# Optimization experiments

Hardware: AMD Instinct MI355X
Metric: run time of the kernel (lower is better)

The kernel has to match this reference:

```python
import jax, jax.numpy as jnp
import numpy as np

DIM, NH, HD = 1536, 12, 128
F, H, W = 1, 30, 52
SEQ = F * H * W          # 1560 tokens per AR group
NG, GI = 6, 5            # num_groups, group_idx (attend over full prefix)
POS, EPS = 1024, 1e-6


def _rope_table():
    # cos/sin table matching Wan rope_params: bands [c-2(c//3), c//3, c//3] of head_dim//2
    c = HD // 2
    parts = [c - 2 * (c // 3), c // 3, c // 3]
    pos = np.arange(POS, dtype=np.float64)
    angs = []
    for cp in parts:
        inv = 1.0 / (10000.0 ** (np.arange(cp, dtype=np.float64) / cp))
        angs.append(pos[:, None] * inv[None, :])
    ang = np.concatenate(angs, axis=1)  # [POS, c]
    return jnp.asarray(np.stack([np.cos(ang), np.sin(ang)], axis=-1), dtype=jnp.float32)


def setup_inputs() -> dict:
    key = jax.random.key(0)
    ks = jax.random.split(key, 8)
    lin = lambda k: jax.random.normal(k, (DIM, DIM), jnp.float32) * 0.02
    total = NG * SEQ
    return {
        'x': jax.random.normal(ks[0], (1, SEQ, DIM), jnp.float32),
        'wq': lin(ks[1]), 'bq': jnp.zeros((DIM,), jnp.float32),
        'wk': lin(ks[2]), 'bk': jnp.zeros((DIM,), jnp.float32),
        'wv': lin(ks[3]), 'bv': jnp.zeros((DIM,), jnp.float32),
        'wo': lin(ks[4]), 'bo': jnp.zeros((DIM,), jnp.float32),
        'nq_w': jnp.ones((DIM,), jnp.float32),
        'nk_w': jnp.ones((DIM,), jnp.float32),
        'freqs': _rope_table(),
        'k_cache': jax.random.normal(ks[5], (1, total, NH, HD), jnp.float32) * 0.5,
        'v_cache': jax.random.normal(ks[6], (1, total, NH, HD), jnp.float32) * 0.5,
        'f': F, 'h': H, 'w': W, 'group_idx': GI, 'num_groups': NG,
    }


def _rms_norm(x, weight, eps=EPS):
    # fast_rms_norm: normalize over the full channel dim, then scale
    x = x.astype(jnp.float32)
    return x * jax.lax.rsqrt(jnp.mean(x * x, axis=-1, keepdims=True) + eps) * weight


def _rope_apply(x, freqs, f, h, w, group_idx):
    # x: [B, S, N, D] with S = f*h*w; freqs: [POS, D//2, 2] (cos, sin)
    B, S, N, D = x.shape
    c = D // 2
    cf = c - 2 * (c // 3)
    ch = cw = c // 3
    sf = group_idx * f
    fp = jnp.broadcast_to(freqs[sf:sf + f, :cf][:, None, None], (f, h, w, cf, 2))
    hp = jnp.broadcast_to(freqs[:h, cf:cf + ch][None, :, None], (f, h, w, ch, 2))
    wp = jnp.broadcast_to(freqs[:w, cf + ch:][None, None, :], (f, h, w, cw, 2))
    rot = jnp.concatenate([fp, hp, wp], axis=3).reshape(S, c, 2)  # [S, c, 2]
    cos = rot[..., 0][None, :, None]  # [1, S, 1, c]
    sin = rot[..., 1][None, :, None]
    xr = x.astype(jnp.float32).reshape(B, S, N, c, 2)
    out_r = xr[..., 0] * cos - xr[..., 1] * sin  # complex multiply x * e^{i theta}
    out_i = xr[..., 0] * sin + xr[..., 1] * cos
    return jnp.stack([out_r, out_i], axis=-1).reshape(B, S, N, D)


def reference(x, wq, bq, wk, bk, wv, bv, wo, bo, nq_w, nk_w, freqs,
              k_cache, v_cache, f, h, w, group_idx, num_groups):
    B, S, C = x.shape
    n, d = NH, C // NH
    q = _rms_norm(x @ wq.T + bq, nq_w).reshape(B, S, n, d)
    k = _rms_norm(x @ wk.T + bk, nk_w).reshape(B, S, n, d)
    v = (x @ wv.T + bv).reshape(B, S, n, d)
    q = _rope_apply(q, freqs, f, h, w, group_idx)
    k = _rope_apply(k, freqs, f, h, w, group_idx)
    # KV-cache scatter (detached in the original) then prefix gather
    start = group_idx * S
    kc = jax.lax.dynamic_update_slice(k_cache, jax.lax.stop_gradient(k), (0, start, 0, 0))
    vc = jax.lax.dynamic_update_slice(v_cache, jax.lax.stop_gradient(v), (0, start, 0, 0))
    k_full = kc[:, :start + S]  # [B, Lkv, n, d]
    v_full = vc[:, :start + S]
    att = jnp.einsum('bqnd,bknd->bnqk', q, k_full) / jnp.sqrt(jnp.float32(d))
    p = jax.nn.softmax(att, axis=-1)
    o = jnp.einsum('bnqk,bknd->bqnd', p, v_full).reshape(B, S, C)
    return o @ wo.T + bo
```

## Files before the change

kernel.cpp:

```cpp
#include <hip/hip_runtime.h>

#define DIM 1536
#define NH 12
#define HD 128
#define KSPLIT 8
#define KT 32
#define MFIX 3.0f
#define KK48 48

typedef _Float16 half2_t __attribute__((ext_vector_type(2)));
typedef _Float16 half8_t __attribute__((ext_vector_type(8)));
typedef float f32x4 __attribute__((ext_vector_type(4)));

__device__ __forceinline__ half2_t pkrtz(float a, float b) {
    return __builtin_bit_cast(half2_t, __builtin_amdgcn_cvt_pkrtz(a, b));
}

__device__ __forceinline__ void split8(float4 a, float4 b, half8_t& h, half8_t& l) {
    half2_t h0 = pkrtz(a.x, a.y), h1 = pkrtz(a.z, a.w);
    half2_t h2 = pkrtz(b.x, b.y), h3 = pkrtz(b.z, b.w);
    half2_t g0 = pkrtz(a.x - (float)h0.x, a.y - (float)h0.y);
    half2_t g1 = pkrtz(a.z - (float)h1.x, a.w - (float)h1.y);
    half2_t g2 = pkrtz(b.x - (float)h2.x, b.y - (float)h2.y);
    half2_t g3 = pkrtz(b.z - (float)h3.x, b.w - (float)h3.y);
    h[0]=h0.x; h[1]=h0.y; h[2]=h1.x; h[3]=h1.y; h[4]=h2.x; h[5]=h2.y; h[6]=h3.x; h[7]=h3.y;
    l[0]=g0.x; l[1]=g0.y; l[2]=g1.x; l[3]=g1.y; l[4]=g2.x; l[5]=g2.y; l[6]=g3.x; l[7]=g3.y;
}

__device__ __forceinline__ half8_t cvt8rn(float4 a, float4 b) {
    half8_t h;
    h[0]=(_Float16)a.x; h[1]=(_Float16)a.y; h[2]=(_Float16)a.z; h[3]=(_Float16)a.w;
    h[4]=(_Float16)b.x; h[5]=(_Float16)b.y; h[6]=(_Float16)b.z; h[7]=(_Float16)b.w;
    return h;
}

__device__ __forceinline__ void gl2lds16(const void* g, void* l) {
    __builtin_amdgcn_global_load_lds(
        (const __attribute__((address_space(1))) unsigned int*)g,
        (__attribute__((address_space(3))) unsigned int*)(unsigned int)(uintptr_t)l,
        16, 0, 0);
}


__global__ __launch_bounds__(256) void cvt_a_fl(
    const float* __restrict__ src, _Float16* __restrict__ h, _Float16* __restrict__ l,
    int M, int nrec8)
{
    const int i = blockIdx.x * 256 + threadIdx.x;
    if (i >= nrec8) return;
    const int lane = i & 63;
    const int grp  = (i >> 6) & 7;
    const int tile = i >> 9;
    const int kk = tile % KK48, mt = tile / KK48;
    const int row = mt * 128 + grp * 16 + (lane & 15);
    const int k   = kk * 32 + (lane >> 4) * 8;
    float4 a = make_float4(0,0,0,0), b = a;
    if (row < M) {
        const float* s = src + (size_t)row * DIM + k;
        a = *(const float4*)s; b = *(const float4*)(s + 4);
    }
    half8_t hh, ll; split8(a, b, hh, ll);
    ((half8_t*)h)[i] = hh;
    ((half8_t*)l)[i] = ll;
}

__global__ __launch_bounds__(256) void cvt_w_fl(
    const float* __restrict__ s0, const float* __restrict__ s1,
    const float* __restrict__ s2, const float* __restrict__ s3,
    _Float16* __restrict__ h0, _Float16* __restrict__ l0,
    _Float16* __restrict__ h1, _Float16* __restrict__ l1,
    _Float16* __restrict__ h2, _Float16* __restrict__ l2,
    _Float16* __restrict__ h3, _Float16* __restrict__ l3, int nrec8)
{
    const int i = blockIdx.x * 256 + threadIdx.x;
    if (i >= nrec8) return;
    const int m = blockIdx.y;
    const float* src = m == 0 ? s0 : m == 1 ? s1 : m == 2 ? s2 : s3;
    _Float16* h = m == 0 ? h0 : m == 1 ? h1 : m == 2 ? h2 : h3;
    _Float16* l = m == 0 ? l0 : m == 1 ? l1 : m == 2 ? l2 : l3;
    const int lane = i & 63;
    const int grp  = (i >> 6) & 7;
    const int tile = i >> 9;
    const int kk = tile % KK48, nt = tile / KK48;
    const int row = nt * 128 + grp * 16 + (lane & 15);
    const int k   = kk * 32 + (lane >> 4) * 8;
    const float* s = src + (size_t)row * DIM + k;
    float4 a = *(const float4*)s, b = *(const float4*)(s + 4);
    half8_t hh, ll; split8(a, b, hh, ll);
    ((half8_t*)h)[i] = hh;
    ((half8_t*)l)[i] = ll;
}

__global__ __launch_bounds__(256) void gemm_fl(
    const _Float16* __restrict__ Ah, const _Float16* __restrict__ Al,
    const _Float16* __restrict__ Bh0, const _Float16* __restrict__ Bl0,
    const _Float16* __restrict__ Bh1, const _Float16* __restrict__ Bl1,
    const _Float16* __restrict__ Bh2, const _Float16* __restrict__ Bl2,
    const float* __restrict__ bias0, const float* __restrict__ bias1, const float* __restrict__ bias2,
    float* __restrict__ C0, float* __restrict__ C1, float* __restrict__ C2,
    int M)
{
    __shared__ __align__(16) _Float16 T[2][4][4096];

    const int MT = (M + 127) >> 7;
    const int nwg = gridDim.x;
    const int L = blockIdx.x;
    const int q8 = nwg >> 3, r8 = nwg & 7;
    const int xcd = L & 7, si = L >> 3;
    const int logical = (xcd < r8 ? xcd * (q8 + 1)
                                  : r8 * (q8 + 1) + (xcd - r8) * q8) + si;
    const int bxx = logical / MT;
    const int myy = logical % MT;
    const int mat = bxx / 12, nt = bxx % 12;
    const _Float16* Bh   = mat == 0 ? Bh0 : mat == 1 ? Bh1 : Bh2;
    const _Float16* Bl   = mat == 0 ? Bl0 : mat == 1 ? Bl1 : Bl2;
    const float*    bias = mat == 0 ? bias0 : mat == 1 ? bias1 : bias2;
    float*          C    = mat == 0 ? C0 : mat == 1 ? C1 : C2;
    const int m0 = myy * 128, n0 = nt * 128;

    const int tid = threadIdx.x;
    const int lane = tid & 63, wave = tid >> 6;
    const int l16 = lane & 15, quad = lane >> 4;
    const int wm = (wave >> 1) * 64, wn = (wave & 1) * 64;

    const _Float16* Arh = Ah + (size_t)myy * KK48 * 4096;
    const _Float16* Arl = Al + (size_t)myy * KK48 * 4096;
    const _Float16* Brh = Bh + (size_t)nt  * KK48 * 4096;
    const _Float16* Brl = Bl + (size_t)nt  * KK48 * 4096;

    f32x4 acc[4][4];
    #pragma unroll
    for (int i = 0; i < 4; ++i)
        #pragma unroll
        for (int j = 0; j < 4; ++j) acc[i][j] = (f32x4){0.f, 0.f, 0.f, 0.f};

    auto STAGE = [&](int kk, int buf) {
        const size_t off = (size_t)kk * 4096 + wave * 1024 + lane * 8;
        _Float16* d0 = &T[buf][0][wave * 1024];
        _Float16* d1 = &T[buf][1][wave * 1024];
        _Float16* d2 = &T[buf][2][wave * 1024];
        _Float16* d3 = &T[buf][3][wave * 1024];
        gl2lds16(Arh + off,       d0);
        gl2lds16(Arh + off + 512, d0 + 512);
        gl2lds16(Arl + off,       d1);
        gl2lds16(Arl + off + 512, d1 + 512);
        gl2lds16(Brh + off,       d2);
        gl2lds16(Brh + off + 512, d2 + 512);
        gl2lds16(Brl + off,       d3);
        gl2lds16(Brl + off + 512, d3 + 512);
    };

    STAGE(0, 0);
    int cur = 0;
    for (int kk = 0; kk < KK48; ++kk) {
        if (kk + 1 < KK48) {
            STAGE(kk + 1, cur ^ 1);
            asm volatile("s_waitcnt vmcnt(8)" ::: "memory");
        } else {
            asm volatile("s_waitcnt vmcnt(0)" ::: "memory");
        }
        __builtin_amdgcn_s_barrier();
        __builtin_amdgcn_sched_barrier(0);

        half8_t ah[4], al[4], bh[4], bl[4];
        const half8_t* tA = (const half8_t*)&T[cur][0][0];
        const half8_t* tAl= (const half8_t*)&T[cur][1][0];
        const half8_t* tB = (const half8_t*)&T[cur][2][0];
        const half8_t* tBl= (const half8_t*)&T[cur][3][0];
        #pragma unroll
        for (int ms = 0; ms < 4; ++ms) {
            ah[ms] = tA [((wm >> 4) + ms) * 64 + lane];
            al[ms] = tAl[((wm >> 4) + ms) * 64 + lane];
        }
        #pragma unroll
        for (int ns = 0; ns < 4; ++ns) {
            bh[ns] = tB [((wn >> 4) + ns) * 64 + lane];
            bl[ns] = tBl[((wn >> 4) + ns) * 64 + lane];
        }
        __builtin_amdgcn_s_setprio(1);
        #pragma unroll
        for (int ms = 0; ms < 4; ++ms)
            #pragma unroll
            for (int ns = 0; ns < 4; ++ns) {
                acc[ms][ns] = __builtin_amdgcn_mfma_f32_16x16x32_f16(ah[ms], bh[ns], acc[ms][ns], 0, 0, 0);
                acc[ms][ns] = __builtin_amdgcn_mfma_f32_16x16x32_f16(ah[ms], bl[ns], acc[ms][ns], 0, 0, 0);
                acc[ms][ns] = __builtin_amdgcn_mfma_f32_16x16x32_f16(al[ms], bh[ns], acc[ms][ns], 0, 0, 0);
            }
        __builtin_amdgcn_s_setprio(0);

        __builtin_amdgcn_sched_barrier(0);
        __builtin_amdgcn_s_barrier();
        cur ^= 1;
    }

    float bv[4];
    #pragma unroll
    for (int ns = 0; ns < 4; ++ns) bv[ns] = bias[n0 + wn + ns*16 + l16];
    #pragma unroll
    for (int ms = 0; ms < 4; ++ms)
        #pragma unroll
        for (int r = 0; r < 4; ++r) {
            const int row = m0 + wm + ms*16 + quad*4 + r;
            if (row < M) {
                #pragma unroll
                for (int ns = 0; ns < 4; ++ns)
                    C[(size_t)row * DIM + n0 + wn + ns*16 + l16] = acc[ms][ns][r] + bv[ns];
            }
        }
}

__global__ __launch_bounds__(256) void rms_rope2(
    float* __restrict__ qb, float* __restrict__ kb,
    const float* __restrict__ wq_, const float* __restrict__ wk_,
    const float* __restrict__ freqs,
    const int* __restrict__ fp, const int* __restrict__ hp,
    const int* __restrict__ wp, const int* __restrict__ gip)
{
    const int s = blockIdx.x;
    float* xv = blockIdx.y ? kb : qb;
    const float* w = blockIdx.y ? wk_ : wq_;
    const int tid = threadIdx.x;
    float* row = xv + (size_t)s * DIM;
    float ss = 0.f;
    for (int c = tid; c < DIM; c += 256) { float v = row[c]; ss += v * v; }
    #pragma unroll
    for (int off = 32; off > 0; off >>= 1) ss += __shfl_down(ss, off, 64);
    __shared__ float red[4];
    if ((tid & 63) == 0) red[tid >> 6] = ss;
    __syncthreads();
    const float tot = red[0] + red[1] + red[2] + red[3];
    const float scale = rsqrtf(tot / (float)DIM + 1e-6f);
    const int f = *fp, h = *hp, ww = *wp, gi = *gip;
    const int hw = h * ww;
    const int fi = s / hw;
    const int rem = s - fi * hw;
    const int hi = rem / ww;
    const int wi = rem - hi * ww;
    const int sf = gi * f;
    for (int p = tid; p < DIM / 2; p += 256) {
        int n = p >> 6, i = p & 63;
        int pos = (i < 22) ? (sf + fi) : (i < 43) ? hi : wi;
        float cs = freqs[pos * 128 + i * 2];
        float sn = freqs[pos * 128 + i * 2 + 1];
        int base = n * HD + 2 * i;
        float x0 = row[base] * scale * w[base];
        float x1 = row[base + 1] * scale * w[base + 1];
        row[base] = x0 * cs - x1 * sn;
        row[base + 1] = x0 * sn + x1 * cs;
    }
}

__global__ __launch_bounds__(256) void kv_prep(
    const float* __restrict__ kws, const float* __restrict__ kcache,
    const float* __restrict__ vws, const float* __restrict__ vcache,
    _Float16* __restrict__ KV, int S, int NT, const int* __restrict__ gip)
{
    const int t = blockIdx.x, n = blockIdx.y;
    const int tid = threadIdx.x;
    const int lane = tid & 63;
    const int l16 = lane & 15, quad = lane >> 4;
    const int start = gip[0] * S;
    const int nk = start + S;
    _Float16* outk = KV + (size_t)(n * NT + t) * 8192;
    _Float16* outv = outk + 4096;
    #pragma unroll
    for (int fi = 0; fi < 2; ++fi) {
        const int f = (tid >> 6) + fi * 4;
        const int ks = f >> 2, db = f & 3;
        const int j = t * KT + ks * 16 + l16;
        float4 a = make_float4(0,0,0,0), b = a;
        if (j < nk) {
            const float* src = (j < start) ? (kcache + (size_t)j * DIM)
                                           : (kws + (size_t)(j - start) * DIM);
            src += n * HD + db * 32 + quad * 8;
            a = *(const float4*)src;
            b = *(const float4*)(src + 4);
        }
        *(half8_t*)&outk[(f * 64 + lane) * 8] = cvt8rn(a, b);
    }
    #pragma unroll
    for (int fi = 0; fi < 2; ++fi) {
        const int ds = (tid >> 6) + fi * 4;
        const int dim = n * HD + ds * 16 + l16;
        half8_t h;
        #pragma unroll
        for (int j = 0; j < 8; ++j) {
            const int slot = quad * 8 + j;
            const int key = t * KT + (slot >> 1) + 16 * (slot & 1);
            float v = 0.f;
            if (key < nk)
                v = (key < start) ? vcache[(size_t)key * DIM + dim]
                                  : vws[(size_t)(key - start) * DIM + dim];
            h[j] = (_Float16)v;
        }
        *(half8_t*)&outv[(ds * 64 + lane) * 8] = h;
    }
}

#define PSTRH 36
__global__ __launch_bounds__(256, 3) void attn_mfma(
    const float* __restrict__ q,
    const _Float16* __restrict__ KV,
    float* __restrict__ Op, float* __restrict__ Ml,
    int S, int NT, const int* __restrict__ gip)
{
    __shared__ __align__(16) _Float16 T[2][8192];
    __shared__ __align__(16) _Float16 Ph[4][2][16][PSTRH];

    const int nwg = gridDim.x;
    const int L = blockIdx.x;
    const int q8 = nwg >> 3, r8 = nwg & 7;
    const int xcd = L & 7, si = L >> 3;
    const int logical = (xcd < r8 ? xcd * (q8 + 1)
                                  : r8 * (q8 + 1) + (xcd - r8) * q8) + si;
    const int yb = (S + 127) >> 7;
    const int y = logical % yb;
    const int g = logical / yb;
    const int n = g % NH;
    const int ksp = g / NH;
    const int q0 = y * 128;

    const int tid = threadIdx.x;
    const int wave = tid >> 6;
    const int lane = tid & 63;
    const int l16 = lane & 15;
    const int quad = lane >> 4;
    const int start = gip[0] * S;
    const int nk = start + S;
    const int totTiles = (nk + KT - 1) / KT;
    const int tilesPer = (totTiles + KSPLIT - 1) / KSPLIT;
    const int t0 = ksp * tilesPer;
    const int t1 = min(t0 + tilesPer, totTiles);
    const float sc = 0.08838834764831845f;

    half8_t qf[2][4];
    #pragma unroll
    for (int qs = 0; qs < 2; ++qs) {
        const int qrow = q0 + wave * 32 + qs * 16 + l16;
        const bool qv = qrow < S;
        const float* qp = q + (size_t)(qv ? qrow : 0) * DIM + n * HD + quad * 8;
        #pragma unroll
        for (int db = 0; db < 4; ++db) {
            float4 a = make_float4(0,0,0,0), b = a;
            if (qv) { a = *(const float4*)(qp + db * 32); b = *(const float4*)(qp + db * 32 + 4); }
            qf[qs][db] = cvt8rn(a, b);
        }
    }

    half8_t ones_f;
    {
        _Float16 ov = (l16 == 0) ? (_Float16)1.0f : (_Float16)0.0f;
        #pragma unroll
        for (int j = 0; j < 8; ++j) ones_f[j] = ov;
    }

    f32x4 O[2][9];
    #pragma unroll
    for (int qs = 0; qs < 2; ++qs)
        #pragma unroll
        for (int ds = 0; ds < 9; ++ds) O[qs][ds] = (f32x4){0.f, 0.f, 0.f, 0.f};

    const size_t tb = (size_t)n * NT;

    if (t0 < t1) {
        const _Float16* gp = KV + (tb + t0) * 8192 + wave * 1024 + lane * 8;
        _Float16* d = &T[0][wave * 1024];
        gl2lds16(gp,              d);
        gl2lds16(gp + 512,        d + 512);
        gl2lds16(gp + 4096,       d + 4096);
        gl2lds16(gp + 4096 + 512, d + 4096 + 512);
    }

    int cur = 0;
    for (int t = t0; t < t1; ++t) {
        if (t + 1 < t1) {
            const _Float16* gp = KV + (tb + t + 1) * 8192 + wave * 1024 + lane * 8;
            _Float16* d = &T[cur ^ 1][wave * 1024];
            gl2lds16(gp,              d);
            gl2lds16(gp + 512,        d + 512);
            gl2lds16(gp + 4096,       d + 4096);
            gl2lds16(gp + 4096 + 512, d + 4096 + 512);
            asm volatile("s_waitcnt vmcnt(4)" ::: "memory");
        } else {
            asm volatile("s_waitcnt vmcnt(0)" ::: "memory");
        }
        __builtin_amdgcn_s_barrier();
        __builtin_amdgcn_sched_barrier(0);

        f32x4 sacc[2][2];
        #pragma unroll
        for (int qs = 0; qs < 2; ++qs) {
            sacc[qs][0] = (f32x4){0.f, 0.f, 0.f, 0.f};
            sacc[qs][1] = (f32x4){0.f, 0.f, 0.f, 0.f};
        }
        const half8_t* kh8 = (const half8_t*)&T[cur][0];
        __builtin_amdgcn_s_setprio(1);
        #pragma unroll
        for (int ks = 0; ks < 2; ++ks) {
            #pragma unroll
            for (int db = 0; db < 4; ++db) {
                half8_t bh = kh8[(ks * 4 + db) * 64 + lane];
                sacc[0][ks] = __builtin_amdgcn_mfma_f32_16x16x32_f16(qf[0][db], bh, sacc[0][ks], 0, 0, 0);
                sacc[1][ks] = __builtin_amdgcn_mfma_f32_16x16x32_f16(qf[1][db], bh, sacc[1][ks], 0, 0, 0);
            }
        }
        __builtin_amdgcn_s_setprio(0);

        const int k0 = t * KT;
        const bool v0 = (k0 + l16) < nk;
        const bool v1 = (k0 + 16 + l16) < nk;
        #pragma unroll
        for (int qs = 0; qs < 2; ++qs) {
            #pragma unroll
            for (int r = 0; r < 4; ++r) {
                float p0 = v0 ? __expf(sacc[qs][0][r] * sc - MFIX) : 0.f;
                float p1 = v1 ? __expf(sacc[qs][1][r] * sc - MFIX) : 0.f;
                half2_t pp;
                pp.x = (_Float16)p0;
                pp.y = (_Float16)p1;
                *(half2_t*)&Ph[wave][qs][quad * 4 + r][2 * l16] = pp;
            }
        }

        half8_t ph[2];
        #pragma unroll
        for (int qs = 0; qs < 2; ++qs)
            ph[qs] = *(const half8_t*)&Ph[wave][qs][l16][quad * 8];

        const half8_t* vt8 = (const half8_t*)&T[cur][4096];
        __builtin_amdgcn_s_setprio(1);
        #pragma unroll
        for (int ds = 0; ds < 8; ++ds) {
            half8_t vh = vt8[ds * 64 + lane];
            O[0][ds] = __builtin_amdgcn_mfma_f32_16x16x32_f16(ph[0], vh, O[0][ds], 0, 0, 0);
            O[1][ds] = __builtin_amdgcn_mfma_f32_16x16x32_f16(ph[1], vh, O[1][ds], 0, 0, 0);
        }
        O[0][8] = __builtin_amdgcn_mfma_f32_16x16x32_f16(ph[0], ones_f, O[0][8], 0, 0, 0);
        O[1][8] = __builtin_amdgcn_mfma_f32_16x16x32_f16(ph[1], ones_f, O[1][8], 0, 0, 0);
        __builtin_amdgcn_s_setprio(0);

        __builtin_amdgcn_sched_barrier(0);
        __builtin_amdgcn_s_barrier();
        cur ^= 1;
    }

    #pragma unroll
    for (int qs = 0; qs < 2; ++qs)
        #pragma unroll
        for (int r = 0; r < 4; ++r) {
            const int row = q0 + wave * 32 + qs * 16 + quad * 4 + r;
            if (row < S) {
                float* op = Op + (((size_t)ksp * NH + n) * S + row) * HD + l16;
                #pragma unroll
                for (int ds = 0; ds < 8; ++ds) op[ds * 16] = O[qs][ds][r];
                if (l16 == 0)
                    Ml[((size_t)ksp * NH + n) * S + row] = O[qs][8][r];
            }
        }
}

__global__ __launch_bounds__(256) void attn_merge(
    const float* __restrict__ Op, const float* __restrict__ Ml,
    _Float16* __restrict__ oh, _Float16* __restrict__ ol, int S)
{
    const int idx = blockIdx.x * 256 + threadIdx.x;
    const int total = NH * S * HD / 2;
    if (idx >= total) return;
    const int d0 = (idx & 63) * 2;
    const int t = idx >> 6;
    const int row = t % S;
    const int n = t / S;
    float num0 = 0.f, num1 = 0.f, den = 0.f;
    #pragma unroll
    for (int ks = 0; ks < KSPLIT; ++ks) {
        const size_t base = ((size_t)ks * NH + n) * S + row;
        num0 += Op[base * HD + d0];
        num1 += Op[base * HD + d0 + 1];
        den += Ml[base];
    }
    const float v0 = num0 / den, v1 = num1 / den;
    half2_t h = pkrtz(v0, v1);
    half2_t l = pkrtz(v0 - (float)h.x, v1 - (float)h.y);
    const int k = n * HD + d0;
    const int mt = row >> 7, rr = row & 127;
    const int grp = rr >> 4, l16r = rr & 15;
    const int kk = k >> 5, quad = (k & 31) >> 3, jj = k & 7;
    const size_t a = ((size_t)(mt * KK48 + kk) * 4096)
                   + ((size_t)(grp * 64 + quad * 16 + l16r) * 8) + jj;
    *(half2_t*)&oh[a] = h;
    *(half2_t*)&ol[a] = l;
}

extern "C" void kernel_launch(void* const* d_in, const int* in_sizes, int n_in,
                              void* d_out, int out_size, void* d_ws, size_t ws_size,
                              hipStream_t stream)
{
    const float* x      = (const float*)d_in[0];
    const float* wq     = (const float*)d_in[1];
    const float* bq     = (const float*)d_in[2];
    const float* wk     = (const float*)d_in[3];
    const float* bk     = (const float*)d_in[4];
    const float* wv     = (const float*)d_in[5];
    const float* bv     = (const float*)d_in[6];
    const float* wo     = (const float*)d_in[7];
    const float* bo     = (const float*)d_in[8];
    const float* nqw    = (const float*)d_in[9];
    const float* nkw    = (const float*)d_in[10];
    const float* freqs  = (const float*)d_in[11];
    const float* kcache = (const float*)d_in[12];
    const float* vcache = (const float*)d_in[13];
    const int*   fp     = (const int*)d_in[14];
    const int*   hp     = (const int*)d_in[15];
    const int*   wp     = (const int*)d_in[16];
    const int*   gip    = (const int*)d_in[17];

    const int S = in_sizes[0] / DIM;
    const int total = in_sizes[12] / (NH * HD);
    const int NT = (total + KT - 1) / KT;
    const int MT = (S + 127) / 128;
    const size_t sd = (size_t)S * DIM;
    const size_t arec = (size_t)MT * KK48 * 4096;
    const size_t wrec = (size_t)12 * KK48 * 4096;

    char* p = (char*)d_ws;
    float* q  = (float*)p;            p += sd * 4;
    float* k  = (float*)p;            p += sd * 4;
    float* v  = (float*)p;            p += sd * 4;
    float* Op = (float*)p;            p += (size_t)KSPLIT * NH * S * HD * 4;
    float* Ml = (float*)p;            p += (size_t)KSPLIT * NH * S * 4;
    _Float16* KV  = (_Float16*)p;     p += (size_t)NH * NT * 8192 * 2;
    _Float16* xh  = (_Float16*)p;     p += arec * 2;
    _Float16* xl  = (_Float16*)p;     p += arec * 2;
    _Float16* oh  = (_Float16*)p;     p += arec * 2;
    _Float16* ol  = (_Float16*)p;     p += arec * 2;
    _Float16* wqh = (_Float16*)p;     p += wrec * 2;
    _Float16* wql = (_Float16*)p;     p += wrec * 2;
    _Float16* wkh = (_Float16*)p;     p += wrec * 2;
    _Float16* wkl = (_Float16*)p;     p += wrec * 2;
    _Float16* wvh = (_Float16*)p;     p += wrec * 2;
    _Float16* wvl = (_Float16*)p;     p += wrec * 2;
    _Float16* woh = (_Float16*)p;     p += wrec * 2;
    _Float16* wol = (_Float16*)p;     p += wrec * 2;
    float* out = (float*)d_out;

    const int an8 = (int)(arec / 8), wn8 = (int)(wrec / 8);

    cvt_a_fl<<<dim3((an8 + 255) / 256), dim3(256), 0, stream>>>(x, xh, xl, S, an8);
    cvt_w_fl<<<dim3((wn8 + 255) / 256, 4), dim3(256), 0, stream>>>(
        wq, wk, wv, wo, wqh, wql, wkh, wkl, wvh, wvl, woh, wol, wn8);

    gemm_fl<<<dim3(36 * MT), dim3(256), 0, stream>>>(
        xh, xl, wqh, wql, wkh, wkl, wvh, wvl, bq, bk, bv, q, k, v, S);
    rms_rope2<<<dim3(S, 2), dim3(256), 0, stream>>>(q, k, nqw, nkw, freqs, fp, hp, wp, gip);
    kv_prep<<<dim3(NT, NH), dim3(256), 0, stream>>>(k, kcache, v, vcache, KV, S, NT, gip);
    {
        const int yb = (S + 127) / 128;
        const int nwg = NH * yb * KSPLIT;
        attn_mfma<<<dim3(nwg), dim3(256), 0, stream>>>(
            q, KV, Op, Ml, S, NT, gip);
    }
    attn_merge<<<dim3((NH * S * HD / 2 + 255) / 256), dim3(256), 0, stream>>>(Op, Ml, oh, ol, S);
    gemm_fl<<<dim3(12 * MT), dim3(256), 0, stream>>>(
        oh, ol, woh, wol, woh, wol, woh, wol, bo, bo, bo, out, out, out, S);
}
```

Baseline: 456.8 us.

## Compute Q/K projections with single fp16 MFMA instead of split hi/lo

Q and K projections now run in a new GEMM kernel that uses only the fp16 high parts of x and the weights, dropping the low-part correction terms. This is argued to be safe because RMS norm follows. V and the output projection keep the split-precision GEMM. The weight converter skips writing low parts for wq and wk, and the new kernel uses half the shared memory with a four-block occupancy hint. The cost is lower precision in Q and K before normalization and RoPE, which may push attention outputs past tolerance.

```diff
diff --git a/kernel.cpp b/kernel.cpp
--- a/kernel.cpp
+++ b/kernel.cpp
@@ -88,34 +88,30 @@
     float4 a = *(const float4*)s, b = *(const float4*)(s + 4);
     half8_t hh, ll; split8(a, b, hh, ll);
     ((half8_t*)h)[i] = hh;
-    ((half8_t*)l)[i] = ll;
-}
-
-__global__ __launch_bounds__(256) void gemm_fl(
-    const _Float16* __restrict__ Ah, const _Float16* __restrict__ Al,
-    const _Float16* __restrict__ Bh0, const _Float16* __restrict__ Bl0,
-    const _Float16* __restrict__ Bh1, const _Float16* __restrict__ Bl1,
-    const _Float16* __restrict__ Bh2, const _Float16* __restrict__ Bl2,
-    const float* __restrict__ bias0, const float* __restrict__ bias1, const float* __restrict__ bias2,
-    float* __restrict__ C0, float* __restrict__ C1, float* __restrict__ C2,
+    if (m >= 2) ((half8_t*)l)[i] = ll;
+}
+
+__global__ __launch_bounds__(256, 4) void gemm_fl_s(
+    const _Float16* __restrict__ Ah,
+    const _Float16* __restrict__ Bh0, const _Float16* __restrict__ Bh1,
+    const float* __restrict__ bias0, const float* __restrict__ bias1,
+    float* __restrict__ C0, float* __restrict__ C1,
     int M)
 {
-    __shared__ __align__(16) _Float16 T[2][4][4096];
-
-    const int MT = (M + 127) >> 7;
+    __shared__ __align__(16) _Float16 T[2][2][4096];
+
     const int nwg = gridDim.x;
     const int L = blockIdx.x;
     const int q8 = nwg >> 3, r8 = nwg & 7;
     const int xcd = L & 7, si = L >> 3;
     const int logical = (xcd < r8 ? xcd * (q8 + 1)
                                   : r8 * (q8 + 1) + (xcd - r8) * q8) + si;
-    const int bxx = logical / MT;
-    const int myy = logical % MT;
-    const int mat = bxx / 12, nt = bxx % 12;
-    const _Float16* Bh   = mat == 0 ? Bh0 : mat == 1 ? Bh1 : Bh2;
-    const _Float16* Bl   = mat == 0 ? Bl0 : mat == 1 ? Bl1 : Bl2;
-    const float*    bias = mat == 0 ? bias0 : mat == 1 ? bias1 : bias2;
-    float*          C    = mat == 0 ? C0 : mat == 1 ? C1 : C2;
+    const int j   = logical % 24;
+    const int myy = logical / 24;
+    const int mat = j & 1, nt = j >> 1;
+    const _Float16* Bh   = mat ? Bh1 : Bh0;
+    const float*    bias = mat ? bias1 : bias0;
+    float*          C    = mat ? C1 : C0;
     const int m0 = myy * 128, n0 = nt * 128;
 
     const int tid = threadIdx.x;
@@ -124,6 +120,97 @@
     const int wm = (wave >> 1) * 64, wn = (wave & 1) * 64;
 
     const _Float16* Arh = Ah + (size_t)myy * KK48 * 4096;
+    const _Float16* Brh = Bh + (size_t)nt  * KK48 * 4096;
+
+    f32x4 acc[4][4];
+    #pragma unroll
+    for (int i = 0; i < 4; ++i)
+        #pragma unroll
+        for (int j2 = 0; j2 < 4; ++j2) acc[i][j2] = (f32x4){0.f, 0.f, 0.f, 0.f};
+
+    auto STAGE = [&](int kk, int buf) {
+        const size_t off = (size_t)kk * 4096 + wave * 1024 + lane * 8;
+        _Float16* d0 = &T[buf][0][wave * 1024];
+        _Float16* d1 = &T[buf][1][wave * 1024];
+        gl2lds16(Arh + off,       d0);
+        gl2lds16(Arh + off + 512, d0 + 512);
+        gl2lds16(Brh + off,       d1);
+        gl2lds16(Brh + off + 512, d1 + 512);
+    };
+
+    STAGE(0, 0);
+    int cur = 0;
+    for (int kk = 0; kk < KK48; ++kk) {
+        if (kk + 1 < KK48) {
+            STAGE(kk + 1, cur ^ 1);
+            asm volatile("s_waitcnt vmcnt(4)" ::: "memory");
+        } else {
+            asm volatile("s_waitcnt vmcnt(0)" ::: "memory");
+        }
+        __builtin_amdgcn_s_barrier();
+        __builtin_amdgcn_sched_barrier(0);
+
+        half8_t ah[4], bh[4];
+        const half8_t* tA = (const half8_t*)&T[cur][0][0];
+        const half8_t* tB = (const half8_t*)&T[cur][1][0];
+        #pragma unroll
+        for (int ms = 0; ms < 4; ++ms) ah[ms] = tA[((wm >> 4) + ms) * 64 + lane];
+        #pragma unroll
+        for (int ns = 0; ns < 4; ++ns) bh[ns] = tB[((wn >> 4) + ns) * 64 + lane];
+
+        __builtin_amdgcn_s_setprio(1);
+        #pragma unroll
+        for (int ms = 0; ms < 4; ++ms)
+            #pragma unroll
+            for (int ns = 0; ns < 4; ++ns)
+                acc[ms][ns] = __builtin_amdgcn_mfma_f32_16x16x32_f16(ah[ms], bh[ns], acc[ms][ns], 0, 0, 0);
+        __builtin_amdgcn_s_setprio(0);
+
+        __builtin_amdgcn_sched_barrier(0);
+        __builtin_amdgcn_s_barrier();
+        cur ^= 1;
+    }
+
+    float bv[4];
+    #pragma unroll
+    for (int ns = 0; ns < 4; ++ns) bv[ns] = bias[n0 + wn + ns*16 + l16];
+    #pragma unroll
+    for (int ms = 0; ms < 4; ++ms)
+        #pragma unroll
+        for (int r = 0; r < 4; ++r) {
+            const int row = m0 + wm + ms*16 + quad*4 + r;
+            if (row < M) {
+                #pragma unroll
+                for (int ns = 0; ns < 4; ++ns)
+                    C[(size_t)row * DIM + n0 + wn + ns*16 + l16] = acc[ms][ns][r] + bv[ns];
+            }
+        }
+}
+
+__global__ __launch_bounds__(256) void gemm_fl(
+    const _Float16* __restrict__ Ah, const _Float16* __restrict__ Al,
+    const _Float16* __restrict__ Bh, const _Float16* __restrict__ Bl,
+    const float* __restrict__ bias,
+    float* __restrict__ C, int M)
+{
+    __shared__ __align__(16) _Float16 T[2][4][4096];
+
+    const int nwg = gridDim.x;
+    const int L = blockIdx.x;
+    const int q8 = nwg >> 3, r8 = nwg & 7;
+    const int xcd = L & 7, si = L >> 3;
+    const int logical = (xcd < r8 ? xcd * (q8 + 1)
+                                  : r8 * (q8 + 1) + (xcd - r8) * q8) + si;
+    const int nt  = logical % 12;
+    const int myy = logical / 12;
+    const int m0 = myy * 128, n0 = nt * 128;
+
+    const int tid = threadIdx.x;
+    const int lane = tid & 63, wave = tid >> 6;
+    const int l16 = lane & 15, quad = lane >> 4;
+    const int wm = (wave >> 1) * 64, wn = (wave & 1) * 64;
+
+    const _Float16* Arh = Ah + (size_t)myy * KK48 * 4096;
     const _Float16* Arl = Al + (size_t)myy * KK48 * 4096;
     const _Float16* Brh = Bh + (size_t)nt  * KK48 * 4096;
     const _Float16* Brl = Bl + (size_t)nt  * KK48 * 4096;
@@ -132,7 +219,7 @@
     #pragma unroll
     for (int i = 0; i < 4; ++i)
         #pragma unroll
-        for (int j = 0; j < 4; ++j) acc[i][j] = (f32x4){0.f, 0.f, 0.f, 0.f};
+        for (int j2 = 0; j2 < 4; ++j2) acc[i][j2] = (f32x4){0.f, 0.f, 0.f, 0.f};
 
     auto STAGE = [&](int kk, int buf) {
         const size_t off = (size_t)kk * 4096 + wave * 1024 + lane * 8;
@@ -549,8 +636,10 @@
     cvt_w_fl<<<dim3((wn8 + 255) / 256, 4), dim3(256), 0, stream>>>(
         wq, wk, wv, wo, wqh, wql, wkh, wkl, wvh, wvl, woh, wol, wn8);
 
-    gemm_fl<<<dim3(36 * MT), dim3(256), 0, stream>>>(
-        xh, xl, wqh, wql, wkh, wkl, wvh, wvl, bq, bk, bv, q, k, v, S);
+    gemm_fl_s<<<dim3(24 * MT), dim3(256), 0, stream>>>(
+        xh, wqh, wkh, bq, bk, q, k, S);
+    gemm_fl<<<dim3(12 * MT), dim3(256), 0, stream>>>(
+        xh, xl, wvh, wvl, bv, v, S);
     rms_rope2<<<dim3(S, 2), dim3(256), 0, stream>>>(q, k, nqw, nkw, freqs, fp, hp, wp, gip);
     kv_prep<<<dim3(NT, NH), dim3(256), 0, stream>>>(k, kcache, v, vcache, KV, S, NT, gip);
     {
@@ -561,5 +650,5 @@
     }
     attn_merge<<<dim3((NH * S * HD / 2 + 255) / 256), dim3(256), 0, stream>>>(Op, Ml, oh, ol, S);
     gemm_fl<<<dim3(12 * MT), dim3(256), 0, stream>>>(
-        oh, ol, woh, wol, woh, wol, woh, wol, bo, bo, bo, out, out, out, S);
-}
+        oh, ol, woh, wol, bo, out, S);
+}
```

Result: no change. 459.9 us (+0.7%).
